# Kernel tuning notes

Measured on AMD Instinct MI355X. Metric: run time of the kernel, lower is better.

## Reference

```python
import jax, jax.numpy as jnp
import numpy as np

NUM_HEADS = 16
KV_GROUPS = 4
MAX_LEN = 2048


def _rope_cos_sin(dim, end, theta=10000.0):
    # precompute_freqs_cis2: dim = head_dim // 2, non-duplicated freqs
    freqs = 1.0 / theta ** (np.arange(0, dim, 2, dtype=np.float32)[: dim // 2] / dim)
    t = np.arange(end, dtype=np.float32)
    f = np.outer(t, freqs)  # [end, dim//2]
    return jnp.asarray(np.cos(f)), jnp.asarray(np.sin(f))


def _apply_cos_sin(x, cos, sin):
    # rotate first half of head_dim with interleaved pairs; second half untouched
    d = x.shape[-1]
    x1, x2 = x[..., : d // 2], x[..., d // 2:]
    x1 = x1.reshape(x1.shape[:-1] + (-1, 2))  # [..., d//4, 2]
    a, b = x1[..., 0], x1[..., 1]
    rot = jnp.stack((a * cos - b * sin, b * cos + a * sin), axis=-1).reshape(x2.shape)
    return jnp.concatenate((rot, x2), axis=-1)


def setup_inputs() -> dict:
    key = jax.random.key(0)
    ks = jax.random.split(key, 9)
    B, S, F = 4, 2048, 2048
    H, G = NUM_HEADS, KV_GROUPS
    Dh = F // H
    sc_q = 1.0 / np.sqrt(F)
    return {
        "x": jax.random.normal(ks[0], (B, S, F), jnp.float32),
        "wq": jax.random.normal(ks[1], (F, H, Dh), jnp.float32) * sc_q,
        "bq": jnp.zeros((H, Dh), jnp.float32),
        "wk": jax.random.normal(ks[2], (F, G, Dh), jnp.float32) * sc_q,
        "bk": jnp.zeros((G, Dh), jnp.float32),
        "wv": jax.random.normal(ks[3], (F, G, Dh), jnp.float32) * sc_q,
        "bv": jnp.zeros((G, Dh), jnp.float32),
        "wo": jax.random.normal(ks[4], (H, Dh, F), jnp.float32) * (1.0 / np.sqrt(F)),
        "bo": jnp.zeros((F,), jnp.float32),
    }


def reference(x, wq, bq, wk, bk, wv, bv, wo, bo):
    B, S, F = x.shape
    H, G = NUM_HEADS, KV_GROUPS
    Dh = F // H

    # QKV projections (DenseGeneral)
    q = jnp.einsum("bsf,fhd->bshd", x, wq) + bq          # [B,S,H,Dh]
    k = jnp.einsum("bsf,fgd->bsgd", x, wk) + bk          # [B,S,G,Dh]
    v = jnp.einsum("bsf,fgd->bsgd", x, wv) + bv

    # GQA: repeat kv groups across query heads
    k = jnp.repeat(k, H // G, axis=2)                    # [B,S,H,Dh]
    v = jnp.repeat(v, H // G, axis=2)

    # RoPE (multi-query variant: partial rotary on first head_dim//2 dims)
    cos, sin = _rope_cos_sin(Dh // 2, MAX_LEN)
    cos_k = cos[None, :S, None, :]
    sin_k = sin[None, :S, None, :]
    q = _apply_cos_sin(q, cos_k, sin_k)
    k = _apply_cos_sin(k, cos_k, sin_k)

    # dot-product attention with causal mask
    scale = 1.0 / jnp.sqrt(jnp.asarray(Dh, x.dtype))
    scores = jnp.einsum("bqhd,bkhd->bhqk", q * scale, k)  # [B,H,S,S]
    causal = jnp.tril(jnp.ones((S, S), bool))
    scores = jnp.where(causal[None, None], scores, jnp.asarray(-1e30, x.dtype))
    probs = jax.nn.softmax(scores, axis=-1)
    attn = jnp.einsum("bhqk,bkhd->bqhd", probs, v)

    # output projection (DenseGeneral over (heads, head_dim))
    return jnp.einsum("bqhd,hdf->bqf", attn, wo) + bo
```

## Files before the change

kernel.cpp:

```cpp
#include <hip/hip_runtime.h>
#include <hip/hip_bf16.h>
#include <math.h>

using bf16 = __hip_bfloat16;
using bf162 = __hip_bfloat162;
typedef __attribute__((ext_vector_type(8))) short frag_ab;
typedef __attribute__((ext_vector_type(4))) float frag_cd;
typedef __attribute__((ext_vector_type(16))) float f32x16;

typedef const __attribute__((address_space(1))) void* gptr_t;
typedef __attribute__((address_space(3))) void* lptr_t;

#define NUM_HEADS 16
#define KV_GROUPS 4
#define SEQ 2048
#define BATCH 4
#define FDIM 2048
#define DH 128
#define NQKV 3072

__global__ __launch_bounds__(256) void cvt_f32_bf16(const float* __restrict__ in,
                                                    bf16* __restrict__ out, int n4) {
  int i = blockIdx.x * 256 + threadIdx.x;
  if (i >= n4) return;
  float4 v = ((const float4*)in)[i];
  bf162 a; a.x = __float2bfloat16(v.x); a.y = __float2bfloat16(v.y);
  bf162 b; b.x = __float2bfloat16(v.z); b.y = __float2bfloat16(v.w);
  ((bf162*)out)[2 * i]     = a;
  ((bf162*)out)[2 * i + 1] = b;
}

__global__ __launch_bounds__(256) void transpose_cvt(const float* __restrict__ src,
                                                     bf16* __restrict__ dst,
                                                     int R, int C) {
  __shared__ float tile[64][65];
  const int ct = blockIdx.x, rt = blockIdx.y;
  const int t = threadIdx.x;
  const int c4 = (t & 15) * 4, r0 = t >> 4;
#pragma unroll
  for (int p = 0; p < 4; p++) {
    int r = r0 + p * 16;
    float4 v = *(const float4*)(src + (size_t)(rt * 64 + r) * C + ct * 64 + c4);
    tile[r][c4] = v.x; tile[r][c4 + 1] = v.y; tile[r][c4 + 2] = v.z; tile[r][c4 + 3] = v.w;
  }
  __syncthreads();
  const int cr = t >> 2, k0 = (t & 3) * 16;
  union { int4 v[2]; bf16 h[16]; } u;
#pragma unroll
  for (int i = 0; i < 16; i++) u.h[i] = __float2bfloat16(tile[k0 + i][cr]);
  bf16* d = dst + (size_t)(ct * 64 + cr) * R + rt * 64 + k0;
  *(int4*)d = u.v[0];
  *(int4*)(d + 8) = u.v[1];
}

template <int OUTBF>
__global__ __launch_bounds__(256) void gemm128(const bf16* __restrict__ A,
                                               const bf16* __restrict__ BT,
                                               void* __restrict__ Cout,
                                               const float* __restrict__ bias,
                                               int M, int N, int K) {
  __shared__ bf16 a_lds[128 * 32];
  __shared__ bf16 b_lds[128 * 32];
  const int tid = threadIdx.x;
  const int wave = tid >> 6, lane = tid & 63;
  const int quad = lane >> 4, l16 = lane & 15;
  const int m0 = blockIdx.x * 128, n0 = blockIdx.y * 128;
  const int wm = (wave & 1) * 64, wn = (wave >> 1) * 64;

  frag_cd acc[4][4];
#pragma unroll
  for (int mt = 0; mt < 4; mt++)
#pragma unroll
    for (int nt = 0; nt < 4; nt++) acc[mt][nt] = (frag_cd){0.f, 0.f, 0.f, 0.f};

  const int seg0 = wave * 64 + lane;
  const int seg1 = (4 + wave) * 64 + lane;
  const bf16* aP0 = A  + (size_t)(m0 + (seg0 >> 2)) * K + (seg0 & 3) * 8;
  const bf16* aP1 = A  + (size_t)(m0 + (seg1 >> 2)) * K + (seg1 & 3) * 8;
  const bf16* bP0 = BT + (size_t)(n0 + (seg0 >> 2)) * K + (seg0 & 3) * 8;
  const bf16* bP1 = BT + (size_t)(n0 + (seg1 >> 2)) * K + (seg1 & 3) * 8;
  bf16* aL0 = &a_lds[(size_t)wave * 64 * 8];
  bf16* aL1 = &a_lds[(size_t)(4 + wave) * 64 * 8];
  bf16* bL0 = &b_lds[(size_t)wave * 64 * 8];
  bf16* bL1 = &b_lds[(size_t)(4 + wave) * 64 * 8];

  for (int k0 = 0; k0 < K; k0 += 32) {
    __syncthreads();
    __builtin_amdgcn_global_load_lds((gptr_t)(aP0 + k0), (lptr_t)aL0, 16, 0, 0);
    __builtin_amdgcn_global_load_lds((gptr_t)(aP1 + k0), (lptr_t)aL1, 16, 0, 0);
    __builtin_amdgcn_global_load_lds((gptr_t)(bP0 + k0), (lptr_t)bL0, 16, 0, 0);
    __builtin_amdgcn_global_load_lds((gptr_t)(bP1 + k0), (lptr_t)bL1, 16, 0, 0);
    __syncthreads();

    frag_ab af[4], bfr[4];
#pragma unroll
    for (int mt = 0; mt < 4; mt++)
      af[mt] = *(const frag_ab*)&a_lds[(wm + mt * 16 + l16) * 32 + quad * 8];
#pragma unroll
    for (int nt = 0; nt < 4; nt++)
      bfr[nt] = *(const frag_ab*)&b_lds[(wn + nt * 16 + l16) * 32 + quad * 8];
#pragma unroll
    for (int mt = 0; mt < 4; mt++)
#pragma unroll
      for (int nt = 0; nt < 4; nt++)
        acc[mt][nt] = __builtin_amdgcn_mfma_f32_16x16x32_bf16(af[mt], bfr[nt], acc[mt][nt], 0, 0, 0);
  }

#pragma unroll
  for (int mt = 0; mt < 4; mt++) {
#pragma unroll
    for (int nt = 0; nt < 4; nt++) {
#pragma unroll
      for (int r = 0; r < 4; r++) {
        int row = m0 + wm + mt * 16 + quad * 4 + r;
        int col = n0 + wn + nt * 16 + l16;
        float v = acc[mt][nt][r];
        if (bias) v += bias[col];
        if (OUTBF) ((bf16*)Cout)[(size_t)row * N + col] = __float2bfloat16(v);
        else       ((float*)Cout)[(size_t)row * N + col] = v;
      }
    }
  }
}

__global__ __launch_bounds__(256) void rope_scatter(const bf16* __restrict__ qkv,
                                                    const float* __restrict__ bq,
                                                    const float* __restrict__ bk,
                                                    const float* __restrict__ bv,
                                                    bf16* __restrict__ Q,
                                                    bf16* __restrict__ K,
                                                    bf16* __restrict__ V) {
  int hrg  = blockIdx.x * 4 + (threadIdx.x >> 6);
  int lane = threadIdx.x & 63;
  int hr  = hrg % 24;
  int row = hrg / 24;
  int b = row >> 11, s = row & 2047;
  int kind, idx;
  if (hr < 16)      { kind = 0; idx = hr; }
  else if (hr < 20) { kind = 1; idx = hr - 16; }
  else              { kind = 2; idx = hr - 20; }
  int colbase = (kind == 0) ? idx * 128 : (kind == 1 ? 2048 + idx * 128 : 2560 + idx * 128);
  const bf16* src = qkv + (size_t)row * NQKV + colbase;
  bf162 xv = *(const bf162*)(src + 2 * lane);
  float a  = __bfloat162float(xv.x);
  float bb = __bfloat162float(xv.y);
  const float* bias = (kind == 0) ? bq : (kind == 1 ? bk : bv);
  a  += bias[idx * 128 + 2 * lane];
  bb += bias[idx * 128 + 2 * lane + 1];
  if (kind != 2 && lane < 32) {
    float freq = powf(10000.f, -(float)lane / 32.f);
    float ang  = (float)s * freq;
    float c = cosf(ang), sn = sinf(ang);
    float na = a * c - bb * sn;
    float nb = bb * c + a * sn;
    a = na; bb = nb;
  }
  if (kind == 0) { a *= 0.08838834764831845f; bb *= 0.08838834764831845f; }
  bf16* dst;
  if (kind == 0)      dst = Q + ((size_t)((b * NUM_HEADS + idx) * SEQ + s)) * DH;
  else if (kind == 1) dst = K + ((size_t)((b * KV_GROUPS + idx) * SEQ + s)) * DH;
  else                dst = V + ((size_t)((b * KV_GROUPS + idx) * SEQ + s)) * DH;
  bf162 ov; ov.x = __float2bfloat16(a); ov.y = __float2bfloat16(bb);
  *(bf162*)(dst + 2 * lane) = ov;
}

__device__ __forceinline__ unsigned pkbf2(float lo, float hi) {
  union { bf16 h[2]; unsigned u; } cv;
  cv.h[0] = __float2bfloat16(lo);
  cv.h[1] = __float2bfloat16(hi);
  return cv.u;
}

__global__ __launch_bounds__(256) void attn_mfma(const bf16* __restrict__ Q,
                                                 const bf16* __restrict__ K,
                                                 const bf16* __restrict__ V,
                                                 bf16* __restrict__ O) {
  __shared__ __align__(16) char smem[32768];
  bf16* k_lds  = (bf16*)smem;
  bf16* vt_lds = (bf16*)(smem + 16384);

  const int tid  = threadIdx.x;
  const int wave = tid >> 6, lane = tid & 63;
  const int l31  = lane & 31, hi = lane >> 5;

  const int bh = blockIdx.x & 63;
  const int t  = 15 - (blockIdx.x >> 6);
  const int h = bh & 15, b = bh >> 4;
  const int grp = h >> 2;
  const int q0 = t * 128;
  const int qa = q0 + wave * 32 + l31;

  const bf16* Qp    = Q + ((size_t)(b * NUM_HEADS + h) * SEQ + qa) * DH;
  const bf16* Kbase = K + (size_t)(b * KV_GROUPS + grp) * SEQ * DH;
  const bf16* Vbase = V + (size_t)(b * KV_GROUPS + grp) * SEQ * DH;

  frag_ab qf[8];
#pragma unroll
  for (int dc = 0; dc < 8; dc++)
    qf[dc] = *(const frag_ab*)(Qp + dc * 16 + hi * 8);

  f32x16 oacc[4];
#pragma unroll
  for (int dbi = 0; dbi < 4; dbi++)
#pragma unroll
    for (int r = 0; r < 16; r++) oacc[dbi][r] = 0.f;
  float m_r = -1e30f, l_r = 0.f;

  const int nkb    = 2 * t + 2;
  const int kblast = 2 * t + (wave >> 1);

  for (int kb = 0; kb < nkb; kb++) {
    __syncthreads();
    const bf16* Kt = Kbase + (size_t)kb * 64 * DH;
#pragma unroll
    for (int i = 0; i < 4; i++) {
      int seg = (i * 4 + wave) * 64 + lane;
      int row = seg >> 4, blk = seg & 15;
      __builtin_amdgcn_global_load_lds(
          (gptr_t)(Kt + (size_t)row * DH + ((blk ^ (row & 15)) << 3)),
          (lptr_t)(k_lds + (i * 4 + wave) * 512), 16, 0, 0);
    }
    const bf16* Vt = Vbase + (size_t)kb * 64 * DH + (size_t)lane * DH + wave * 32;
#pragma unroll
    for (int i = 0; i < 4; i++) {
      union { int4 v; bf16 hh[8]; } u;
      u.v = *(const int4*)(Vt + i * 8);
#pragma unroll
      for (int s = 0; s < 8; s++) {
        int d = wave * 32 + i * 8 + s;
        vt_lds[d * 64 + (((lane * 2) ^ ((d & 7) << 4)) >> 1)] = u.hh[s];
      }
    }
    __syncthreads();

    if (kb <= kblast) {
      f32x16 sacc[2];
#pragma unroll
      for (int c = 0; c < 2; c++)
#pragma unroll
        for (int r = 0; r < 16; r++) sacc[c][r] = 0.f;
#pragma unroll
      for (int kc = 0; kc < 2; kc++) {
        const int krow = kc * 32 + l31;
        const int sw = (krow & 15) << 4;
#pragma unroll
        for (int dc = 0; dc < 8; dc++) {
          frag_ab kf = *(const frag_ab*)&k_lds[krow * 128 + (((dc * 32 + hi * 16) ^ sw) >> 1)];
          sacc[kc] = __builtin_amdgcn_mfma_f32_32x32x16_bf16(kf, qf[dc], sacc[kc], 0, 0, 0);
        }
      }
      if (kb == kblast) {
        const int kb64 = kb * 64 + 4 * hi;
#pragma unroll
        for (int c = 0; c < 2; c++)
#pragma unroll
          for (int r = 0; r < 16; r++) {
            int k = kb64 + c * 32 + (r & 3) + 8 * (r >> 2);
            if (k > qa) sacc[c][r] = -1e30f;
          }
      }
      float mx = -1e30f;
#pragma unroll
      for (int c = 0; c < 2; c++)
#pragma unroll
        for (int r = 0; r < 16; r++) mx = fmaxf(mx, sacc[c][r]);
      mx = fmaxf(mx, __shfl_xor(mx, 32));
      float mnew = fmaxf(m_r, mx);
      float alpha = __expf(m_r - mnew);
      float ps = 0.f;
#pragma unroll
      for (int c = 0; c < 2; c++)
#pragma unroll
        for (int r = 0; r < 16; r++) {
          float p = __expf(sacc[c][r] - mnew);
          sacc[c][r] = p;
          ps += p;
        }
      ps += __shfl_xor(ps, 32);
      m_r = mnew;
      l_r = l_r * alpha + ps;
#pragma unroll
      for (int dbi = 0; dbi < 4; dbi++)
#pragma unroll
        for (int r = 0; r < 16; r++) oacc[dbi][r] *= alpha;

      frag_ab pa[4];
#pragma unroll
      for (int c = 0; c < 2; c++)
#pragma unroll
        for (int ks = 0; ks < 2; ks++) {
          unsigned z0 = pkbf2(sacc[c][8 * ks + 0], sacc[c][8 * ks + 1]);
          unsigned z1 = pkbf2(sacc[c][8 * ks + 2], sacc[c][8 * ks + 3]);
          unsigned z2 = pkbf2(sacc[c][8 * ks + 4], sacc[c][8 * ks + 5]);
          unsigned z3 = pkbf2(sacc[c][8 * ks + 6], sacc[c][8 * ks + 7]);
          unsigned s0 = (unsigned)__shfl_xor((int)z0, 32);
          unsigned s1 = (unsigned)__shfl_xor((int)z1, 32);
          unsigned s2 = (unsigned)__shfl_xor((int)z2, 32);
          unsigned s3 = (unsigned)__shfl_xor((int)z3, 32);
          union { unsigned u[4]; frag_ab f; } w;
          w.u[0] = hi ? s2 : z0;
          w.u[1] = hi ? s3 : z1;
          w.u[2] = hi ? z2 : s0;
          w.u[3] = hi ? z3 : s1;
          pa[c * 2 + ks] = w.f;
        }
#pragma unroll
      for (int dbi = 0; dbi < 4; dbi++) {
        const int d = dbi * 32 + l31;
        const int sw = (d & 7) << 4;
#pragma unroll
        for (int ks = 0; ks < 4; ks++) {
          frag_ab vf = *(const frag_ab*)&vt_lds[d * 64 + (((ks * 32 + hi * 16) ^ sw) >> 1)];
          oacc[dbi] = __builtin_amdgcn_mfma_f32_32x32x16_bf16(vf, pa[ks], oacc[dbi], 0, 0, 0);
        }
      }
    }
  }

  __syncthreads();
  const float invl = 1.f / l_r;
  const int qrow = wave * 32 + l31;
#pragma unroll
  for (int dbi = 0; dbi < 4; dbi++)
#pragma unroll
    for (int i = 0; i < 8; i++) {
      int dd = ((2 * i) & 3) + 8 * (i >> 1) + 4 * hi;
      unsigned pv = pkbf2(oacc[dbi][2 * i] * invl, oacc[dbi][2 * i + 1] * invl);
      int colb = (dbi * 32 + dd) * 2;
      *(unsigned*)(smem + qrow * 256 + (colb ^ ((qrow & 15) << 4))) = pv;
    }
  __syncthreads();
  const int rr = tid >> 1, hf = tid & 1;
  bf16* Op = O + (size_t)(b * SEQ + q0 + rr) * FDIM + h * DH + hf * 64;
#pragma unroll
  for (int i = 0; i < 8; i++) {
    int colb = hf * 128 + i * 16;
    int4 v = *(const int4*)(smem + rr * 256 + (colb ^ ((rr & 15) << 4)));
    *(int4*)(Op + i * 8) = v;
  }
}

extern "C" void kernel_launch(void* const* d_in, const int* in_sizes, int n_in,
                              void* d_out, int out_size, void* d_ws, size_t ws_size,
                              hipStream_t stream) {
  const float* x  = (const float*)d_in[0];
  const float* wq = (const float*)d_in[1];
  const float* bq = (const float*)d_in[2];
  const float* wk = (const float*)d_in[3];
  const float* bk = (const float*)d_in[4];
  const float* wv = (const float*)d_in[5];
  const float* bv = (const float*)d_in[6];
  const float* wo = (const float*)d_in[7];
  const float* bo = (const float*)d_in[8];
  float* out = (float*)d_out;

  char* ws = (char*)d_ws;
  size_t off = 0;
  auto alloc = [&](size_t bytes) {
    void* p = ws + off;
    off += (bytes + 255) & ~(size_t)255;
    return p;
  };
  const size_t MS = (size_t)BATCH * SEQ;
  bf16* Xb    = (bf16*)alloc(MS * FDIM * 2);
  bf16* WqkvT = (bf16*)alloc((size_t)NQKV * FDIM * 2);
  bf16* WoT   = (bf16*)alloc((size_t)FDIM * FDIM * 2);
  bf16* QKV   = (bf16*)alloc(MS * NQKV * 2);
  bf16* Qb    = (bf16*)alloc((size_t)BATCH * NUM_HEADS * SEQ * DH * 2);
  bf16* Kb    = (bf16*)alloc((size_t)BATCH * KV_GROUPS * SEQ * DH * 2);
  bf16* Vb    = (bf16*)alloc((size_t)BATCH * KV_GROUPS * SEQ * DH * 2);
  bf16* Ob    = (bf16*)alloc(MS * FDIM * 2);

  int n4x = (int)(MS * FDIM / 4);
  cvt_f32_bf16<<<(n4x + 255) / 256, 256, 0, stream>>>(x, Xb, n4x);

  transpose_cvt<<<dim3(2048 / 64, 2048 / 64), 256, 0, stream>>>(wq, WqkvT, 2048, 2048);
  transpose_cvt<<<dim3(512 / 64, 2048 / 64), 256, 0, stream>>>(wk, WqkvT + (size_t)2048 * 2048, 2048, 512);
  transpose_cvt<<<dim3(512 / 64, 2048 / 64), 256, 0, stream>>>(wv, WqkvT + (size_t)2560 * 2048, 2048, 512);
  transpose_cvt<<<dim3(2048 / 64, 2048 / 64), 256, 0, stream>>>(wo, WoT, 2048, 2048);

  dim3 g1(MS / 128, NQKV / 128);
  gemm128<1><<<g1, 256, 0, stream>>>(Xb, WqkvT, QKV, nullptr, (int)MS, NQKV, FDIM);

  rope_scatter<<<(int)(MS * 24 / 4), 256, 0, stream>>>(QKV, bq, bk, bv, Qb, Kb, Vb);

  attn_mfma<<<dim3(64 * 16), 256, 0, stream>>>(Qb, Kb, Vb, Ob);

  dim3 g2(MS / 128, FDIM / 128);
  gemm128<0><<<g2, 256, 0, stream>>>(Ob, WoT, out, bo, (int)MS, FDIM, FDIM);
}
```

Baseline: 674.5 us.

## Pre-transpose V globally and skip online-softmax rescale when max barely grows

Adds a transpose_v kernel that writes V as [bg][d][seq]. The attention kernel can then stage V^T tiles into LDS with async global_load_lds, like K, instead of doing per-element scattered LDS stores. It also makes the online-softmax rescale lazy: the running max and the O/l accumulators are only rescaled when some lane's block max exceeds the running max by more than 8. This trades an extra kernel launch and an extra V round trip through memory for cheaper LDS staging and fewer rescale multiplies, at the cost of slightly larger exp ranges.

```diff
diff --git a/kernel.cpp b/kernel.cpp
--- a/kernel.cpp
+++ b/kernel.cpp
@@ -51,6 +51,32 @@
   bf16* d = dst + (size_t)(ct * 64 + cr) * R + rt * 64 + k0;
   *(int4*)d = u.v[0];
   *(int4*)(d + 8) = u.v[1];
+}
+
+__global__ __launch_bounds__(256) void transpose_v(const bf16* __restrict__ Vb,
+                                                   bf16* __restrict__ VT) {
+  __shared__ bf16 tile[64][136];
+  const int kt = blockIdx.x, bg = blockIdx.y;
+  const int t = threadIdx.x;
+  const int key = t >> 2, c4 = t & 3;
+  const bf16* src = Vb + ((size_t)bg * SEQ + kt * 64 + key) * DH + c4 * 32;
+#pragma unroll
+  for (int p = 0; p < 4; p++) {
+    union { int4 v; bf16 hh[8]; } u;
+    u.v = *(const int4*)(src + p * 8);
+#pragma unroll
+    for (int j = 0; j < 8; j++) tile[key][c4 * 32 + p * 8 + j] = u.hh[j];
+  }
+  __syncthreads();
+  const int dt = t >> 3, kb8 = t & 7;
+#pragma unroll
+  for (int p2 = 0; p2 < 4; p2++) {
+    int d = p2 * 32 + dt;
+    union { int4 v; bf16 hh[8]; } u;
+#pragma unroll
+    for (int j = 0; j < 8; j++) u.hh[j] = tile[kb8 * 8 + j][d];
+    *(int4*)(VT + ((size_t)bg * DH + d) * SEQ + kt * 64 + kb8 * 8) = u.v;
+  }
 }
 
 template <int OUTBF>
@@ -173,7 +199,7 @@
 
 __global__ __launch_bounds__(256) void attn_mfma(const bf16* __restrict__ Q,
                                                  const bf16* __restrict__ K,
-                                                 const bf16* __restrict__ V,
+                                                 const bf16* __restrict__ VT,
                                                  bf16* __restrict__ O) {
   __shared__ __align__(16) char smem[32768];
   bf16* k_lds  = (bf16*)smem;
@@ -190,9 +216,9 @@
   const int q0 = t * 128;
   const int qa = q0 + wave * 32 + l31;
 
-  const bf16* Qp    = Q + ((size_t)(b * NUM_HEADS + h) * SEQ + qa) * DH;
-  const bf16* Kbase = K + (size_t)(b * KV_GROUPS + grp) * SEQ * DH;
-  const bf16* Vbase = V + (size_t)(b * KV_GROUPS + grp) * SEQ * DH;
+  const bf16* Qp     = Q  + ((size_t)(b * NUM_HEADS + h) * SEQ + qa) * DH;
+  const bf16* Kbase  = K  + (size_t)(b * KV_GROUPS + grp) * SEQ * DH;
+  const bf16* VTbase = VT + (size_t)(b * KV_GROUPS + grp) * DH * SEQ;
 
   frag_ab qf[8];
 #pragma unroll
@@ -218,18 +244,15 @@
       int row = seg >> 4, blk = seg & 15;
       __builtin_amdgcn_global_load_lds(
           (gptr_t)(Kt + (size_t)row * DH + ((blk ^ (row & 15)) << 3)),
-          (lptr_t)(k_lds + (i * 4 + wave) * 512), 16, 0, 0);
+          (lptr_t)(k_lds + seg * 8), 16, 0, 0);
     }
-    const bf16* Vt = Vbase + (size_t)kb * 64 * DH + (size_t)lane * DH + wave * 32;
 #pragma unroll
     for (int i = 0; i < 4; i++) {
-      union { int4 v; bf16 hh[8]; } u;
-      u.v = *(const int4*)(Vt + i * 8);
-#pragma unroll
-      for (int s = 0; s < 8; s++) {
-        int d = wave * 32 + i * 8 + s;
-        vt_lds[d * 64 + (((lane * 2) ^ ((d & 7) << 4)) >> 1)] = u.hh[s];
-      }
+      int seg = (i * 4 + wave) * 64 + lane;
+      int d = seg >> 3, blk = seg & 7;
+      __builtin_amdgcn_global_load_lds(
+          (gptr_t)(VTbase + (size_t)d * SEQ + kb * 64 + ((blk ^ (d & 7)) << 3)),
+          (lptr_t)(vt_lds + seg * 8), 16, 0, 0);
     }
     __syncthreads();
 
@@ -265,24 +288,27 @@
 #pragma unroll
         for (int r = 0; r < 16; r++) mx = fmaxf(mx, sacc[c][r]);
       mx = fmaxf(mx, __shfl_xor(mx, 32));
-      float mnew = fmaxf(m_r, mx);
-      float alpha = __expf(m_r - mnew);
+      if (__any(mx > m_r + 8.f)) {
+        float mnew = fmaxf(m_r, mx);
+        float alpha = __expf(m_r - mnew);
+        l_r *= alpha;
+#pragma unroll
+        for (int dbi = 0; dbi < 4; dbi++)
+#pragma unroll
+          for (int r = 0; r < 16; r++) oacc[dbi][r] *= alpha;
+        m_r = mnew;
+      }
       float ps = 0.f;
 #pragma unroll
       for (int c = 0; c < 2; c++)
 #pragma unroll
         for (int r = 0; r < 16; r++) {
-          float p = __expf(sacc[c][r] - mnew);
+          float p = __expf(sacc[c][r] - m_r);
           sacc[c][r] = p;
           ps += p;
         }
       ps += __shfl_xor(ps, 32);
-      m_r = mnew;
-      l_r = l_r * alpha + ps;
-#pragma unroll
-      for (int dbi = 0; dbi < 4; dbi++)
-#pragma unroll
-        for (int r = 0; r < 16; r++) oacc[dbi][r] *= alpha;
+      l_r += ps;
 
       frag_ab pa[4];
 #pragma unroll
@@ -369,6 +395,7 @@
   bf16* Qb    = (bf16*)alloc((size_t)BATCH * NUM_HEADS * SEQ * DH * 2);
   bf16* Kb    = (bf16*)alloc((size_t)BATCH * KV_GROUPS * SEQ * DH * 2);
   bf16* Vb    = (bf16*)alloc((size_t)BATCH * KV_GROUPS * SEQ * DH * 2);
+  bf16* VTb   = (bf16*)alloc((size_t)BATCH * KV_GROUPS * DH * SEQ * 2);
   bf16* Ob    = (bf16*)alloc(MS * FDIM * 2);
 
   int n4x = (int)(MS * FDIM / 4);
@@ -384,7 +411,9 @@
 
   rope_scatter<<<(int)(MS * 24 / 4), 256, 0, stream>>>(QKV, bq, bk, bv, Qb, Kb, Vb);
 
-  attn_mfma<<<dim3(64 * 16), 256, 0, stream>>>(Qb, Kb, Vb, Ob);
+  transpose_v<<<dim3(SEQ / 64, BATCH * KV_GROUPS), 256, 0, stream>>>(Vb, VTb);
+
+  attn_mfma<<<dim3(64 * 16), 256, 0, stream>>>(Qb, Kb, VTb, Ob);
 
   dim3 g2(MS / 128, FDIM / 128);
   gemm128<0><<<g2, 256, 0, stream>>>(Ob, WoT, out, bo, (int)MS, FDIM, FDIM);
```

Result: faster. 644.9 us (-4.4%).
